# Performance work log

Hardware: AMD Instinct MI355X
Metric: run time of the kernel (lower is better)

The kernel has to match this reference:

```python
import jax, jax.numpy as jnp
import numpy as np

B, OBS, D, V = 32, 768, 512, 64  # batch, obs_dim, latent/action/embed dim, max_vars


def _gelu(x):
    return jax.nn.gelu(x, approximate=False)  # torch nn.GELU default is exact erf


def setup_inputs() -> dict:
    key = jax.random.key(0)
    ks = jax.random.split(key, 16)
    s = lambda k, shape, scale=0.02: (jax.random.normal(k, shape, jnp.float32) * scale)
    return {
        "obs": jax.random.normal(ks[0], (B, OBS), jnp.float32),
        "action": jax.random.normal(ks[1], (B, D), jnp.float32),
        # CausalGraphLearner params
        "embed": jax.random.normal(ks[2], (V, D), jnp.float32),  # nn.Embedding weight
        "sc_w1": s(ks[3], (2 * D, 3 * D)), "sc_b1": jnp.zeros((2 * D,), jnp.float32),
        "sc_w2": s(ks[4], (1, 2 * D)), "sc_b2": jnp.zeros((1,), jnp.float32),
        # WorldModelEngine params
        "enc_w1": s(ks[5], (2 * D, OBS)), "enc_b1": jnp.zeros((2 * D,), jnp.float32),
        "enc_w2": s(ks[6], (D, 2 * D)), "enc_b2": jnp.zeros((D,), jnp.float32),
        "gru_wih": s(ks[7], (3 * D, 2 * D)), "gru_whh": s(ks[8], (3 * D, D)),
        "gru_bih": jnp.zeros((3 * D,), jnp.float32), "gru_bhh": jnp.zeros((3 * D,), jnp.float32),
        "dec_w": s(ks[9], (OBS, D)), "dec_b": jnp.zeros((OBS,), jnp.float32),
        # reasoner params
        "rs_w1": s(ks[10], (D, D)), "rs_b1": jnp.zeros((D,), jnp.float32),
        "rs_w2": s(ks[11], (D, D)), "rs_b2": jnp.zeros((D,), jnp.float32),
    }


def reference(obs, action, embed, sc_w1, sc_b1, sc_w2, sc_b2,
              enc_w1, enc_b1, enc_w2, enc_b2,
              gru_wih, gru_whh, gru_bih, gru_bhh,
              dec_w, dec_b, rs_w1, rs_b1, rs_w2, rs_b2):
    # --- WorldModelEngine ---
    z = _gelu(obs @ enc_w1.T + enc_b1) @ enc_w2.T + enc_b2            # [B, D]
    x = jnp.concatenate([z, action], axis=-1)                          # [B, 2D]
    h0 = jnp.zeros((obs.shape[0], D), obs.dtype)                       # h=None -> zeros
    gi = x @ gru_wih.T + gru_bih                                       # [B, 3D]
    gh = h0 @ gru_whh.T + gru_bhh                                      # [B, 3D]
    r = jax.nn.sigmoid(gi[:, :D] + gh[:, :D])
    u = jax.nn.sigmoid(gi[:, D:2 * D] + gh[:, D:2 * D])
    n = jnp.tanh(gi[:, 2 * D:] + r * gh[:, 2 * D:])
    h = (1.0 - u) * n + u * h0                                         # [B, D]
    pred = h @ dec_w.T + dec_b                                         # [B, OBS]

    # --- CausalGraphLearner ---
    # Linear-of-concat identity: W1 @ cat(cause, effect, ctx) = Wa@cause + Wb@effect + Wc@ctx
    Wa, Wb, Wc = sc_w1[:, :D], sc_w1[:, D:2 * D], sc_w1[:, 2 * D:]
    Ea = embed @ Wa.T                                                  # [V, 2D]
    Eb = embed @ Wb.T                                                  # [V, 2D]
    Cc = (h + action) @ Wc.T                                           # [B, 2D]
    hid = _gelu(Cc[:, None, None, :] + Ea[None, :, None, :]
                + Eb[None, None, :, :] + sc_b1)                        # [B, V, V, 2D]
    scores = jax.nn.sigmoid(jnp.einsum('bijd,d->bij', hid, sc_w2[0]) + sc_b2[0])  # [B,V,V]
    graph = scores.mean(0)                                             # [V, V] (returned scores)

    # --- reasoner ---
    reasoning = _gelu(h @ rs_w1.T + rs_b1) @ rs_w2.T + rs_b2           # [B, D]

    return (h, pred, graph, reasoning)
```

## Files before the change

kernel.cpp:

```cpp
#include <hip/hip_runtime.h>
#include <math.h>


#if __has_builtin(__builtin_amdgcn_exp2f)
#define EXP2F __builtin_amdgcn_exp2f
#else
#define EXP2F exp2f
#endif

__device__ __forceinline__ float gelu_exact(float x) {
    return 0.5f * x * (1.f + erff(x * 0.70710678118654752f));
}
__device__ __forceinline__ float sigmoid_fast(float v) {
    return __builtin_amdgcn_rcpf(1.f + EXP2F(-1.442695041f * v));
}
__device__ __forceinline__ float tanh_fast(float v) {
    return fmaf(-2.f, __builtin_amdgcn_rcpf(1.f + EXP2F(2.885390082f * v)), 1.f);
}

template<int NF4, int ACT, int BT>
__device__ __forceinline__ void wgemm(int wid,
        const float* __restrict__ A, int lda,
        const float* __restrict__ W, int ldw,
        const float* __restrict__ bias,
        float* __restrict__ out, int ldo,
        int oblocks) {
    int lane = threadIdx.x & 63;
    int oblock = wid % oblocks;
    int bgroup = wid / oblocks;
    int o0 = oblock * 8, b0 = bgroup * BT;

    float4 w[8][NF4];
#pragma unroll
    for (int r = 0; r < 8; ++r) {
        const float4* wr = reinterpret_cast<const float4*>(W + (o0 + r) * ldw);
#pragma unroll
        for (int c = 0; c < NF4; ++c) w[r][c] = wr[c * 64 + lane];
    }
    float bv = bias ? bias[o0 + (lane & 7)] : 0.f;
    bool p0 = lane & 1, p1 = lane & 2, p2 = lane & 4;

#pragma unroll
    for (int bi = 0; bi < BT; ++bi) {
        const float4* ar = reinterpret_cast<const float4*>(A + (b0 + bi) * lda);
        float4 a[NF4];
#pragma unroll
        for (int c = 0; c < NF4; ++c) a[c] = ar[c * 64 + lane];
        float s[8];
#pragma unroll
        for (int r = 0; r < 8; ++r) {
            float acc = 0.f;
#pragma unroll
            for (int c = 0; c < NF4; ++c) {
                acc = fmaf(a[c].x, w[r][c].x, acc);
                acc = fmaf(a[c].y, w[r][c].y, acc);
                acc = fmaf(a[c].z, w[r][c].z, acc);
                acc = fmaf(a[c].w, w[r][c].w, acc);
            }
            s[r] = acc;
        }
        float m[4];
#pragma unroll
        for (int k = 0; k < 4; ++k) {
            float keep = p0 ? s[2 * k + 1] : s[2 * k];
            float send = p0 ? s[2 * k] : s[2 * k + 1];
            m[k] = keep + __shfl_xor(send, 1, 64);
        }
        float n[2];
#pragma unroll
        for (int k = 0; k < 2; ++k) {
            float keep = p1 ? m[2 * k + 1] : m[2 * k];
            float send = p1 ? m[2 * k] : m[2 * k + 1];
            n[k] = keep + __shfl_xor(send, 2, 64);
        }
        float F;
        {
            float keep = p2 ? n[1] : n[0];
            float send = p2 ? n[0] : n[1];
            F = keep + __shfl_xor(send, 4, 64);
        }
        F += __shfl_xor(F, 8, 64);
        F += __shfl_xor(F, 16, 64);
        F += __shfl_xor(F, 32, 64);
        float v = F + bv;
        if (ACT) v = gelu_exact(v);
        if (lane < 8) out[(b0 + bi) * ldo + o0 + lane] = v;
    }
}

__global__ void __launch_bounds__(256) front_kernel(
    const float* __restrict__ obs, const float* __restrict__ enc_w1,
    const float* __restrict__ enc_b1, float* __restrict__ h1,
    const float* __restrict__ embed, const float* __restrict__ sc_w1,
    const float* __restrict__ sc_b1, float* __restrict__ Ea, float* __restrict__ Eb,
    const float* __restrict__ action, const float* __restrict__ wih,
    const float* __restrict__ bih, float* __restrict__ gia) {
    int wid = blockIdx.x * 4 + (threadIdx.x >> 6);
    if (wid < 1024) {
        wgemm<3, 1, 4>(wid, obs, 768, enc_w1, 768, enc_b1, h1, 1024, 128);
    } else if (wid < 3072) {
        wgemm<2, 0, 4>(wid - 1024, embed, 512, sc_w1, 1536, sc_b1, Ea, 1024, 128);
    } else if (wid < 5120) {
        wgemm<2, 0, 4>(wid - 3072, embed, 512, sc_w1 + 512, 1536, nullptr, Eb, 1024, 128);
    } else {
        wgemm<2, 0, 4>(wid - 5120, action, 512, wih + 512, 1024, bih, gia, 1536, 192);
    }
}

__global__ void __launch_bounds__(256) enc2_kernel(
    const float* __restrict__ h1, const float* __restrict__ enc_w2,
    const float* __restrict__ enc_b2, float* __restrict__ z) {
    int wid = blockIdx.x * 4 + (threadIdx.x >> 6);
    wgemm<4, 0, 2>(wid, h1, 1024, enc_w2, 1024, enc_b2, z, 512, 64);
}

__global__ void __launch_bounds__(256) gigru_kernel(
    const float* __restrict__ z, const float* __restrict__ wih,
    const float* __restrict__ gia, const float* __restrict__ bhh,
    const float* __restrict__ action, float* __restrict__ h, float* __restrict__ ha) {
    int wid = blockIdx.x * 4 + (threadIdx.x >> 6);
    int lane = threadIdx.x & 63;
    int opair = wid & 255;
    int bg = wid >> 8;
    int o0 = opair * 2, b0 = bg * 2;

    int rows[6] = {o0, o0 + 1, 512 + o0, 513 + o0, 1024 + o0, 1025 + o0};
    float4 w[6][2];
#pragma unroll
    for (int r = 0; r < 6; ++r) {
        const float4* wr = reinterpret_cast<const float4*>(wih + rows[r] * 1024);
#pragma unroll
        for (int c = 0; c < 2; ++c) w[r][c] = wr[c * 64 + lane];
    }
    float bhr0 = bhh[o0],        bhr1 = bhh[o0 + 1];
    float bhu0 = bhh[512 + o0],  bhu1 = bhh[513 + o0];
    float bhn0 = bhh[1024 + o0], bhn1 = bhh[1025 + o0];

#pragma unroll
    for (int bi = 0; bi < 2; ++bi) {
        int b = b0 + bi;
        const float4* ar = reinterpret_cast<const float4*>(z + b * 512);
        float4 a[2] = {ar[lane], ar[64 + lane]};
        float s[6];
#pragma unroll
        for (int r = 0; r < 6; ++r) {
            float acc = 0.f;
#pragma unroll
            for (int c = 0; c < 2; ++c) {
                acc = fmaf(a[c].x, w[r][c].x, acc);
                acc = fmaf(a[c].y, w[r][c].y, acc);
                acc = fmaf(a[c].z, w[r][c].z, acc);
                acc = fmaf(a[c].w, w[r][c].w, acc);
            }
            s[r] = acc;
        }
#pragma unroll
        for (int m = 1; m < 64; m <<= 1) {
#pragma unroll
            for (int r = 0; r < 6; ++r) s[r] += __shfl_xor(s[r], m, 64);
        }
        if (lane == 0) {
            const float* gb = gia + b * 1536;
            float r0 = sigmoid_fast(s[0] + gb[o0]        + bhr0);
            float r1 = sigmoid_fast(s[1] + gb[o0 + 1]    + bhr1);
            float u0 = sigmoid_fast(s[2] + gb[512 + o0]  + bhu0);
            float u1 = sigmoid_fast(s[3] + gb[513 + o0]  + bhu1);
            float n0 = tanh_fast(s[4] + gb[1024 + o0] + r0 * bhn0);
            float n1 = tanh_fast(s[5] + gb[1025 + o0] + r1 * bhn1);
            float hv0 = (1.f - u0) * n0;
            float hv1 = (1.f - u1) * n1;
            h[b * 512 + o0]      = hv0;
            h[b * 512 + o0 + 1]  = hv1;
            ha[b * 512 + o0]     = hv0 + action[b * 512 + o0];
            ha[b * 512 + o0 + 1] = hv1 + action[b * 512 + o0 + 1];
        }
    }
}

__global__ void __launch_bounds__(256) mid_kernel(
    const float* __restrict__ h, const float* __restrict__ ha,
    const float* __restrict__ dec_w, const float* __restrict__ dec_b, float* __restrict__ pred,
    const float* __restrict__ rs_w1, const float* __restrict__ rs_b1, float* __restrict__ r1,
    const float* __restrict__ sc_w1, float* __restrict__ Cc) {
    int wid = blockIdx.x * 4 + (threadIdx.x >> 6);
    if (wid < 1536) {
        wgemm<2, 0, 2>(wid, h, 512, dec_w, 512, dec_b, pred, 768, 96);
    } else if (wid < 2560) {
        wgemm<2, 1, 2>(wid - 1536, h, 512, rs_w1, 512, rs_b1, r1, 512, 64);
    } else {
        wgemm<2, 0, 2>(wid - 2560, ha, 512, sc_w1 + 1024, 1536, nullptr, Cc, 1024, 128);
    }
}

__global__ void __launch_bounds__(256) score_rs2_kernel(
    const float* __restrict__ Ea, const float* __restrict__ Eb,
    const float* __restrict__ Cc, const float* __restrict__ w2,
    const float* __restrict__ b2, float* __restrict__ graph,
    const float* __restrict__ r1, const float* __restrict__ rs_w2,
    const float* __restrict__ rs_b2, float* __restrict__ reasoning) {
    int blk = blockIdx.x;
    if (blk < 64) {
        int wid = blk * 4 + (threadIdx.x >> 6);
        wgemm<2, 0, 8>(wid, r1, 512, rs_w2, 512, rs_b2, reasoning, 512, 64);
    }
    int i = blk >> 5;
    int j0 = (blk & 31) << 1;
    int lane = threadIdx.x & 63;
    int wave = threadIdx.x >> 6;
    int d0 = lane << 4;

    const float4* Ea4  = reinterpret_cast<const float4*>(Ea + i * 1024 + d0);
    const float4* Eb04 = reinterpret_cast<const float4*>(Eb + j0 * 1024 + d0);
    const float4* Eb14 = reinterpret_cast<const float4*>(Eb + (j0 + 1) * 1024 + d0);
    const float4* W4   = reinterpret_cast<const float4*>(w2 + d0);

    const float NK = -2.4554274f;
    float basea[16], df[16], g[16], wv[16];
#pragma unroll
    for (int c = 0; c < 4; ++c) {
        float4 e  = Ea4[c];
        float4 f0 = Eb04[c];
        float4 f1 = Eb14[c];
        float4 w  = W4[c];
        basea[4 * c + 0] = e.x + f0.x; basea[4 * c + 1] = e.y + f0.y;
        basea[4 * c + 2] = e.z + f0.z; basea[4 * c + 3] = e.w + f0.w;
        df[4 * c + 0] = f1.x - f0.x; df[4 * c + 1] = f1.y - f0.y;
        df[4 * c + 2] = f1.z - f0.z; df[4 * c + 3] = f1.w - f0.w;
        wv[4 * c + 0] = w.x; wv[4 * c + 1] = w.y;
        wv[4 * c + 2] = w.z; wv[4 * c + 3] = w.w;
    }
#pragma unroll
    for (int e = 0; e < 16; ++e) g[e] = EXP2F(df[e] * NK);

    float sA[8], sB[8];
#pragma unroll
    for (int b = 0; b < 8; ++b) { sA[b] = 0.f; sB[b] = 0.f; }

    const float* ccbase = Cc + (wave * 8) * 1024 + d0;
#pragma unroll
    for (int b = 0; b < 8; ++b) {
        const float4* q4 = reinterpret_cast<const float4*>(ccbase + b * 1024);
        float4 c0 = q4[0], c1 = q4[1], c2 = q4[2], c3 = q4[3];
        float cc[16] = {c0.x, c0.y, c0.z, c0.w, c1.x, c1.y, c1.z, c1.w,
                        c2.x, c2.y, c2.z, c2.w, c3.x, c3.y, c3.z, c3.w};
#pragma unroll
        for (int e = 0; e < 16; e += 2) {
            float xa0 = cc[e] + basea[e];
            float xa1 = cc[e + 1] + basea[e + 1];
            float ta0 = EXP2F(xa0 * NK);
            float ta1 = EXP2F(xa1 * NK);
            float da0 = 1.f + ta0, da1 = 1.f + ta1;
            float numa = fmaf(xa0 * wv[e], da1, (xa1 * wv[e + 1]) * da0);
            float P = da0 * da1;

            float xb0 = xa0 + df[e];
            float xb1 = xa1 + df[e + 1];
            float tb0 = ta0 * g[e];
            float tb1 = ta1 * g[e + 1];
            float db0 = 1.f + tb0, db1 = 1.f + tb1;
            float numb = fmaf(xb0 * wv[e], db1, (xb1 * wv[e + 1]) * db0);
            float Q = db0 * db1;

            float R = __builtin_amdgcn_rcpf(P * Q);
            sA[b] = fmaf(numa * Q, R, sA[b]);
            sB[b] = fmaf(numb * P, R, sB[b]);
        }
    }

    bool p0 = lane & 1, p1 = lane & 2, p2 = lane & 4, p3 = lane & 8;
    float m[8];
#pragma unroll
    for (int k = 0; k < 8; ++k) {
        float keep = p0 ? sB[k] : sA[k];
        float send = p0 ? sA[k] : sB[k];
        m[k] = keep + __shfl_xor(send, 1, 64);
    }
    float n[4];
#pragma unroll
    for (int k = 0; k < 4; ++k) {
        float keep = p1 ? m[2 * k + 1] : m[2 * k];
        float send = p1 ? m[2 * k] : m[2 * k + 1];
        n[k] = keep + __shfl_xor(send, 2, 64);
    }
    float o2[2];
#pragma unroll
    for (int k = 0; k < 2; ++k) {
        float keep = p2 ? n[2 * k + 1] : n[2 * k];
        float send = p2 ? n[2 * k] : n[2 * k + 1];
        o2[k] = keep + __shfl_xor(send, 4, 64);
    }
    float F;
    {
        float keep = p3 ? o2[1] : o2[0];
        float send = p3 ? o2[0] : o2[1];
        F = keep + __shfl_xor(send, 8, 64);
    }
    F += __shfl_xor(F, 16, 64);
    F += __shfl_xor(F, 32, 64);

    float sig = sigmoid_fast(F + b2[0]);
    sig += __shfl_xor(sig, 2, 64);
    sig += __shfl_xor(sig, 4, 64);
    sig += __shfl_xor(sig, 8, 64);

    __shared__ float red[4][2];
    if (lane < 2) red[wave][lane] = sig;
    __syncthreads();
    if (threadIdx.x < 2) {
        graph[i * 64 + j0 + threadIdx.x] =
            (red[0][threadIdx.x] + red[1][threadIdx.x] +
             red[2][threadIdx.x] + red[3][threadIdx.x]) * 0.03125f;
    }
}

extern "C" void kernel_launch(void* const* d_in, const int* in_sizes, int n_in,
                              void* d_out, int out_size, void* d_ws, size_t ws_size,
                              hipStream_t stream) {
    const float* obs     = (const float*)d_in[0];
    const float* action  = (const float*)d_in[1];
    const float* embed   = (const float*)d_in[2];
    const float* sc_w1   = (const float*)d_in[3];
    const float* sc_b1   = (const float*)d_in[4];
    const float* sc_w2   = (const float*)d_in[5];
    const float* sc_b2   = (const float*)d_in[6];
    const float* enc_w1  = (const float*)d_in[7];
    const float* enc_b1  = (const float*)d_in[8];
    const float* enc_w2  = (const float*)d_in[9];
    const float* enc_b2  = (const float*)d_in[10];
    const float* gru_wih = (const float*)d_in[11];
    const float* gru_bih = (const float*)d_in[13];
    const float* gru_bhh = (const float*)d_in[14];
    const float* dec_w   = (const float*)d_in[15];
    const float* dec_b   = (const float*)d_in[16];
    const float* rs_w1   = (const float*)d_in[17];
    const float* rs_b1   = (const float*)d_in[18];
    const float* rs_w2   = (const float*)d_in[19];
    const float* rs_b2   = (const float*)d_in[20];

    float* ws = (float*)d_ws;
    float* h1  = ws + 0;
    float* z   = ws + 32768;
    float* gia = ws + 49152;
    float* ha  = ws + 98304;
    float* r1  = ws + 114688;
    float* Cc  = ws + 131072;
    float* Ea  = ws + 163840;
    float* Eb  = ws + 229376;

    float* h_out     = (float*)d_out;
    float* pred      = h_out + 16384;
    float* graph     = h_out + 40960;
    float* reasoning = h_out + 45056;

    front_kernel<<<1664, 256, 0, stream>>>(obs, enc_w1, enc_b1, h1,
                                           embed, sc_w1, sc_b1, Ea, Eb,
                                           action, gru_wih, gru_bih, gia);
    enc2_kernel<<<256, 256, 0, stream>>>(h1, enc_w2, enc_b2, z);
    gigru_kernel<<<1024, 256, 0, stream>>>(z, gru_wih, gia, gru_bhh, action, h_out, ha);
    mid_kernel<<<1152, 256, 0, stream>>>(h_out, ha, dec_w, dec_b, pred,
                                         rs_w1, rs_b1, r1, sc_w1, Cc);
    score_rs2_kernel<<<2048, 256, 0, stream>>>(Ea, Eb, Cc, sc_w2, sc_b2, graph,
                                               r1, rs_w2, rs_b2, reasoning);
}
```

Baseline: 165.4 us.

## Move decoder GEMM into score kernel and restructure score reduction loop

The decoder projection (pred) moves out of mid_kernel and into score_rs2_kernel, where it runs on blocks 64-159 alongside the reasoner's second layer. This shrinks mid_kernel's grid and overlaps the decoder work with the score computation. The score loop is now rolled, with the next batch row of Cc prefetched into registers, and each batch row is reduced by a full wave butterfly rather than a transposed multi-level reduction. This is meant to cut register pressure, but it adds many more shuffles per block.

```diff
diff --git a/kernel.cpp b/kernel.cpp
--- a/kernel.cpp
+++ b/kernel.cpp
@@ -179,16 +179,13 @@
 
 __global__ void __launch_bounds__(256) mid_kernel(
     const float* __restrict__ h, const float* __restrict__ ha,
-    const float* __restrict__ dec_w, const float* __restrict__ dec_b, float* __restrict__ pred,
     const float* __restrict__ rs_w1, const float* __restrict__ rs_b1, float* __restrict__ r1,
     const float* __restrict__ sc_w1, float* __restrict__ Cc) {
     int wid = blockIdx.x * 4 + (threadIdx.x >> 6);
-    if (wid < 1536) {
-        wgemm<2, 0, 2>(wid, h, 512, dec_w, 512, dec_b, pred, 768, 96);
-    } else if (wid < 2560) {
-        wgemm<2, 1, 2>(wid - 1536, h, 512, rs_w1, 512, rs_b1, r1, 512, 64);
+    if (wid < 1024) {
+        wgemm<2, 1, 2>(wid, h, 512, rs_w1, 512, rs_b1, r1, 512, 64);
     } else {
-        wgemm<2, 0, 2>(wid - 2560, ha, 512, sc_w1 + 1024, 1536, nullptr, Cc, 1024, 128);
+        wgemm<2, 0, 2>(wid - 1024, ha, 512, sc_w1 + 1024, 1536, nullptr, Cc, 1024, 128);
     }
 }
 
@@ -197,16 +194,21 @@
     const float* __restrict__ Cc, const float* __restrict__ w2,
     const float* __restrict__ b2, float* __restrict__ graph,
     const float* __restrict__ r1, const float* __restrict__ rs_w2,
-    const float* __restrict__ rs_b2, float* __restrict__ reasoning) {
+    const float* __restrict__ rs_b2, float* __restrict__ reasoning,
+    const float* __restrict__ h, const float* __restrict__ dec_w,
+    const float* __restrict__ dec_b, float* __restrict__ pred) {
     int blk = blockIdx.x;
+    int lane = threadIdx.x & 63;
+    int wave = threadIdx.x >> 6;
     if (blk < 64) {
-        int wid = blk * 4 + (threadIdx.x >> 6);
+        int wid = blk * 4 + wave;
         wgemm<2, 0, 8>(wid, r1, 512, rs_w2, 512, rs_b2, reasoning, 512, 64);
+    } else if (blk < 160) {
+        int wid = (blk - 64) * 4 + wave;
+        wgemm<2, 0, 8>(wid, h, 512, dec_w, 512, dec_b, pred, 768, 96);
     }
     int i = blk >> 5;
     int j0 = (blk & 31) << 1;
-    int lane = threadIdx.x & 63;
-    int wave = threadIdx.x >> 6;
     int d0 = lane << 4;
 
     const float4* Ea4  = reinterpret_cast<const float4*>(Ea + i * 1024 + d0);
@@ -232,17 +234,20 @@
 #pragma unroll
     for (int e = 0; e < 16; ++e) g[e] = EXP2F(df[e] * NK);
 
-    float sA[8], sB[8];
-#pragma unroll
-    for (int b = 0; b < 8; ++b) { sA[b] = 0.f; sB[b] = 0.f; }
-
+    float keepA = 0.f, keepB = 0.f;
     const float* ccbase = Cc + (wave * 8) * 1024 + d0;
-#pragma unroll
+    const float4* q0 = reinterpret_cast<const float4*>(ccbase);
+    float4 m0 = q0[0], m1 = q0[1], m2 = q0[2], m3 = q0[3];
+
+#pragma unroll 1
     for (int b = 0; b < 8; ++b) {
-        const float4* q4 = reinterpret_cast<const float4*>(ccbase + b * 1024);
-        float4 c0 = q4[0], c1 = q4[1], c2 = q4[2], c3 = q4[3];
-        float cc[16] = {c0.x, c0.y, c0.z, c0.w, c1.x, c1.y, c1.z, c1.w,
-                        c2.x, c2.y, c2.z, c2.w, c3.x, c3.y, c3.z, c3.w};
+        float cc[16] = {m0.x, m0.y, m0.z, m0.w, m1.x, m1.y, m1.z, m1.w,
+                        m2.x, m2.y, m2.z, m2.w, m3.x, m3.y, m3.z, m3.w};
+        if (b < 7) {
+            const float4* qn = reinterpret_cast<const float4*>(ccbase + (b + 1) * 1024);
+            m0 = qn[0]; m1 = qn[1]; m2 = qn[2]; m3 = qn[3];
+        }
+        float s0 = 0.f, s1 = 0.f;
 #pragma unroll
         for (int e = 0; e < 16; e += 2) {
             float xa0 = cc[e] + basea[e];
@@ -262,49 +267,29 @@
             float Q = db0 * db1;
 
             float R = __builtin_amdgcn_rcpf(P * Q);
-            sA[b] = fmaf(numa * Q, R, sA[b]);
-            sB[b] = fmaf(numb * P, R, sB[b]);
-        }
-    }
-
-    bool p0 = lane & 1, p1 = lane & 2, p2 = lane & 4, p3 = lane & 8;
-    float m[8];
-#pragma unroll
-    for (int k = 0; k < 8; ++k) {
-        float keep = p0 ? sB[k] : sA[k];
-        float send = p0 ? sA[k] : sB[k];
-        m[k] = keep + __shfl_xor(send, 1, 64);
-    }
-    float n[4];
-#pragma unroll
-    for (int k = 0; k < 4; ++k) {
-        float keep = p1 ? m[2 * k + 1] : m[2 * k];
-        float send = p1 ? m[2 * k] : m[2 * k + 1];
-        n[k] = keep + __shfl_xor(send, 2, 64);
-    }
-    float o2[2];
-#pragma unroll
-    for (int k = 0; k < 2; ++k) {
-        float keep = p2 ? n[2 * k + 1] : n[2 * k];
-        float send = p2 ? n[2 * k] : n[2 * k + 1];
-        o2[k] = keep + __shfl_xor(send, 4, 64);
-    }
-    float F;
-    {
-        float keep = p3 ? o2[1] : o2[0];
-        float send = p3 ? o2[0] : o2[1];
-        F = keep + __shfl_xor(send, 8, 64);
-    }
-    F += __shfl_xor(F, 16, 64);
-    F += __shfl_xor(F, 32, 64);
-
-    float sig = sigmoid_fast(F + b2[0]);
-    sig += __shfl_xor(sig, 2, 64);
-    sig += __shfl_xor(sig, 4, 64);
-    sig += __shfl_xor(sig, 8, 64);
+            s0 = fmaf(numa * Q, R, s0);
+            s1 = fmaf(numb * P, R, s1);
+        }
+#pragma unroll
+        for (int mm = 1; mm < 64; mm <<= 1) {
+            s0 += __shfl_xor(s0, mm, 64);
+            s1 += __shfl_xor(s1, mm, 64);
+        }
+        keepA = (lane == b) ? s0 : keepA;
+        keepB = (lane == b) ? s1 : keepB;
+    }
+
+    float bsc = b2[0];
+    float sigA = (lane < 8) ? sigmoid_fast(keepA + bsc) : 0.f;
+    float sigB = (lane < 8) ? sigmoid_fast(keepB + bsc) : 0.f;
+#pragma unroll
+    for (int mm = 1; mm < 8; mm <<= 1) {
+        sigA += __shfl_xor(sigA, mm, 64);
+        sigB += __shfl_xor(sigB, mm, 64);
+    }
 
     __shared__ float red[4][2];
-    if (lane < 2) red[wave][lane] = sig;
+    if (lane == 0) { red[wave][0] = sigA; red[wave][1] = sigB; }
     __syncthreads();
     if (threadIdx.x < 2) {
         graph[i * 64 + j0 + threadIdx.x] =
@@ -357,8 +342,8 @@
                                            action, gru_wih, gru_bih, gia);
     enc2_kernel<<<256, 256, 0, stream>>>(h1, enc_w2, enc_b2, z);
     gigru_kernel<<<1024, 256, 0, stream>>>(z, gru_wih, gia, gru_bhh, action, h_out, ha);
-    mid_kernel<<<1152, 256, 0, stream>>>(h_out, ha, dec_w, dec_b, pred,
-                                         rs_w1, rs_b1, r1, sc_w1, Cc);
+    mid_kernel<<<768, 256, 0, stream>>>(h_out, ha, rs_w1, rs_b1, r1, sc_w1, Cc);
     score_rs2_kernel<<<2048, 256, 0, stream>>>(Ea, Eb, Cc, sc_w2, sc_b2, graph,
-                                               r1, rs_w2, rs_b2, reasoning);
-}
+                                               r1, rs_w2, rs_b2, reasoning,
+                                               h_out, dec_w, dec_b, pred);
+}
```

Measured after the change: 169.6 us. +2.5%, slower.
